# Optimization experiments

Hardware: AMD Instinct MI355X
Metric: run time of the kernel (lower is better)

The kernel has to match this reference:

```python
import jax, jax.numpy as jnp
import numpy as np

B, S, D_IN, D_HID, D_LAT = 64, 1024, 256, 512, 128
GRU_DIMS = [D_LAT, 256, 128]
D_OUT = 2
EPS_BN = 1e-5
EPS_LN = 1e-5


def _lin(key, out_d, in_d):
    k1, k2 = jax.random.split(key)
    s = 1.0 / np.sqrt(in_d)
    return (jax.random.uniform(k1, (out_d, in_d), jnp.float32, -s, s),
            jax.random.uniform(k2, (out_d,), jnp.float32, -s, s))


def setup_inputs() -> dict:
    key = jax.random.key(0)
    ks = jax.random.split(key, 16)
    x = jax.random.normal(ks[0], (B, S, D_IN), jnp.float32)
    eps = jax.random.normal(ks[1], (B, S, D_LAT), jnp.float32)
    W1lv, b1lv = _lin(ks[2], D_HID, D_IN)
    W2lv, b2lv = _lin(ks[3], D_LAT, D_HID)
    Wmu, bmu = _lin(ks[4], D_LAT, D_IN)
    Wdec, bdec = _lin(ks[5], D_IN, D_LAT)
    # GRU layer 0: in=128 -> hid=256; layer 1: in=256 -> hid=128
    Wih0, bih0 = _lin(ks[6], 3 * GRU_DIMS[1], GRU_DIMS[0])
    Whh0, bhh0 = _lin(ks[7], 3 * GRU_DIMS[1], GRU_DIMS[1])
    Wih1, bih1 = _lin(ks[8], 3 * GRU_DIMS[2], GRU_DIMS[1])
    Whh1, bhh1 = _lin(ks[9], 3 * GRU_DIMS[2], GRU_DIMS[2])
    fc_W, fc_b = _lin(ks[10], D_OUT, GRU_DIMS[2])
    return dict(
        x=x, eps=eps,
        W1lv=W1lv, b1lv=b1lv, W2lv=W2lv, b2lv=b2lv, Wmu=Wmu, bmu=bmu,
        bn_g=jnp.ones((D_LAT,), jnp.float32), bn_b=jnp.zeros((D_LAT,), jnp.float32),
        bn_rm=jnp.zeros((D_LAT,), jnp.float32), bn_rv=jnp.ones((D_LAT,), jnp.float32),
        Wdec=Wdec, bdec=bdec,
        Wih0=Wih0, Whh0=Whh0, bih0=bih0, bhh0=bhh0,
        Wih1=Wih1, Whh1=Whh1, bih1=bih1, bhh1=bhh1,
        ln_g0=jnp.ones((GRU_DIMS[1],), jnp.float32), ln_b0=jnp.zeros((GRU_DIMS[1],), jnp.float32),
        ln_g1=jnp.ones((GRU_DIMS[2],), jnp.float32), ln_b1=jnp.zeros((GRU_DIMS[2],), jnp.float32),
        fc_W=fc_W, fc_b=fc_b,
    )


def _gru_cell(x, h, Wih, Whh, bih, bhh):
    gi = x @ Wih.T + bih                      # [B, 3H]
    gh = h @ Whh.T + bhh
    ir, iz, inn = jnp.split(gi, 3, axis=-1)
    hr, hz, hn = jnp.split(gh, 3, axis=-1)
    r = jax.nn.sigmoid(ir + hr)
    zg = jax.nn.sigmoid(iz + hz)
    n = jnp.tanh(inn + r * hn)
    return (1.0 - zg) * n + zg * h


def _layernorm(h, g, b):
    m = jnp.mean(h, axis=-1, keepdims=True)
    v = jnp.var(h, axis=-1, keepdims=True)
    return (h - m) * jax.lax.rsqrt(v + EPS_LN) * g + b


def reference(x, eps, W1lv, b1lv, W2lv, b2lv, Wmu, bmu, bn_g, bn_b, bn_rm, bn_rv,
              Wdec, bdec, Wih0, Whh0, bih0, bhh0, Wih1, Whh1, bih1, bhh1,
              ln_g0, ln_b0, ln_g1, ln_b1, fc_W, fc_b):
    # --- Encoder ---
    xl = jnp.log(jax.nn.softplus(x))                       # [B,S,D_IN]
    h_enc = jax.nn.relu(xl @ W1lv.T + b1lv)                # [B,S,D_HID]
    logvar = h_enc @ W2lv.T + b2lv                         # [B,S,D_LAT]
    mu = xl @ Wmu.T + bmu                                  # [B,S,D_LAT]
    # BatchNorm1d over latent channel (eval mode, running stats)
    mu = (mu - bn_rm) * jax.lax.rsqrt(bn_rv + EPS_BN) * bn_g + bn_b
    mu = jnp.clip(mu, -10.0, 10.0)
    # --- Reparameterize ---
    z = mu + eps * jnp.exp(0.5 * logvar)                   # [B,S,D_LAT]
    # --- Decoder ---
    x_recon = jnp.exp(z @ Wdec.T + bdec)                   # [B,S,D_IN]
    # --- Stacked GRUCell + LayerNorm over time ---
    batch = x.shape[0]
    h0 = jnp.zeros((batch, GRU_DIMS[1]), z.dtype)
    h1 = jnp.zeros((batch, GRU_DIMS[2]), z.dtype)

    def step(carry, z_t):
        h0, h1 = carry
        h0 = _layernorm(_gru_cell(z_t, h0, Wih0, Whh0, bih0, bhh0), ln_g0, ln_b0)
        h1 = _layernorm(_gru_cell(h0, h1, Wih1, Whh1, bih1, bhh1), ln_g1, ln_b1)
        return (h0, h1), None

    (h0, h1), _ = jax.lax.scan(step, (h0, h1), jnp.swapaxes(z, 0, 1))
    # fc head (dropout is identity in eval mode); output_series=False
    v = h1 @ fc_W.T + fc_b                                 # [B, D_OUT]
    return (v, x_recon, mu, logvar)
```

## Files before the change

### kernel.cpp

```cpp
#include <hip/hip_runtime.h>
#include <cstdint>

#define TOKENS 65536

#define WS_XL    0ULL
#define WS_HENC  67108864ULL
#define WS_GI0   0ULL
#define WS_XBUF0 201326592ULL
#define WS_XBUF1 (201326592ULL + 131072ULL)
#define WS_CNT   (201326592ULL + 196608ULL)
#define WS_MUS   (201326592ULL + 229376ULL)
#define WS_MUT   (201326592ULL + 229888ULL)
#define WS_NEED  (201326592ULL + 230400ULL)
#define CNT_STRIDE 64

__global__ void k_prep(const float* __restrict__ bmu, const float* __restrict__ bng,
                       const float* __restrict__ bnb, const float* __restrict__ bnrm,
                       const float* __restrict__ bnrv,
                       float* __restrict__ mus, float* __restrict__ mut)
{
    int j = threadIdx.x;
    if (j < 128) {
        float s = bng[j] / sqrtf(bnrv[j] + 1e-5f);
        mus[j] = s;
        mut[j] = bmu[j] * s + bnb[j] - bnrm[j] * s;
    }
}

__global__ void k_xl(const float* __restrict__ x, float* __restrict__ xl, int n4)
{
    int i = blockIdx.x * blockDim.x + threadIdx.x;
    if (i >= n4) return;
    float4 v = ((const float4*)x)[i];
    float4 o;
    o.x = logf(v.x > 20.f ? v.x : log1pf(expf(v.x)));
    o.y = logf(v.y > 20.f ? v.y : log1pf(expf(v.y)));
    o.z = logf(v.z > 20.f ? v.z : log1pf(expf(v.z)));
    o.w = logf(v.w > 20.f ? v.w : log1pf(expf(v.w)));
    ((float4*)xl)[i] = o;
}

template<int EPI, int AZ>
__global__ __launch_bounds__(256) void k_gemm_f32(
    const float* __restrict__ A, const float* __restrict__ W,
    const float* __restrict__ svec, const float* __restrict__ tvec,
    float* __restrict__ C, int N, int K,
    const float* __restrict__ ZMU, const float* __restrict__ ZLV, const float* __restrict__ ZEP)
{
    __shared__ float As[32][132];
    __shared__ float Ws[32][132];
    const int tid = threadIdx.x;
    const int tx = tid & 15, ty = tid >> 4;
    const int m0 = blockIdx.x * 128;
    const int n0 = blockIdx.y * 128;
    float acc[8][8];
#pragma unroll
    for (int i = 0; i < 8; ++i)
#pragma unroll
        for (int j = 0; j < 8; ++j) acc[i][j] = 0.f;

    for (int k0 = 0; k0 < K; k0 += 32) {
#pragma unroll
        for (int it = 0; it < 4; ++it) {
            int id = tid + 256 * it;
            int r = id >> 3, c4 = id & 7;
            float4 av;
            if constexpr (AZ) {
                size_t idx = (size_t)(m0 + r) * K + k0 + c4 * 4;
                float4 m4 = *(const float4*)(ZMU + idx);
                float4 l4 = *(const float4*)(ZLV + idx);
                float4 e4 = *(const float4*)(ZEP + idx);
                av.x = m4.x + e4.x * expf(0.5f * l4.x);
                av.y = m4.y + e4.y * expf(0.5f * l4.y);
                av.z = m4.z + e4.z * expf(0.5f * l4.z);
                av.w = m4.w + e4.w * expf(0.5f * l4.w);
            } else {
                av = *(const float4*)(A + (size_t)(m0 + r) * K + k0 + c4 * 4);
            }
            float4 wv = *(const float4*)(W + (size_t)(n0 + r) * K + k0 + c4 * 4);
            As[c4*4+0][r] = av.x; As[c4*4+1][r] = av.y; As[c4*4+2][r] = av.z; As[c4*4+3][r] = av.w;
            Ws[c4*4+0][r] = wv.x; Ws[c4*4+1][r] = wv.y; Ws[c4*4+2][r] = wv.z; Ws[c4*4+3][r] = wv.w;
        }
        __syncthreads();
#pragma unroll
        for (int k = 0; k < 32; ++k) {
            float4 a0 = *(const float4*)&As[k][ty*8];
            float4 a1 = *(const float4*)&As[k][ty*8+4];
            float4 w0 = *(const float4*)&Ws[k][tx*8];
            float4 w1 = *(const float4*)&Ws[k][tx*8+4];
            float ar[8] = {a0.x,a0.y,a0.z,a0.w,a1.x,a1.y,a1.z,a1.w};
            float wr[8] = {w0.x,w0.y,w0.z,w0.w,w1.x,w1.y,w1.z,w1.w};
#pragma unroll
            for (int i = 0; i < 8; ++i)
#pragma unroll
                for (int j = 0; j < 8; ++j) acc[i][j] += ar[i] * wr[j];
        }
        __syncthreads();
    }
#pragma unroll
    for (int i = 0; i < 8; ++i) {
        size_t m = (size_t)m0 + ty*8 + i;
#pragma unroll
        for (int j4 = 0; j4 < 2; ++j4) {
            float o[4];
#pragma unroll
            for (int j = 0; j < 4; ++j) {
                int col = n0 + tx*8 + j4*4 + j;
                float v = acc[i][j4*4+j];
                if (svec) v *= svec[col];
                v += tvec[col];
                if constexpr (EPI == 1) v = fmaxf(v, 0.f);
                if constexpr (EPI == 2) v = fminf(fmaxf(v, -10.f), 10.f);
                if constexpr (EPI == 3) v = expf(v);
                o[j] = v;
            }
            *(float4*)(C + m * N + n0 + tx*8 + j4*4) = *(float4*)o;
        }
    }
}

__device__ __forceinline__ void xstore(float* p, float v) {
    __hip_atomic_store(p, v, __ATOMIC_RELAXED, __HIP_MEMORY_SCOPE_AGENT);
}
__device__ __forceinline__ float xload(const float* p) {
    return __hip_atomic_load(p, __ATOMIC_RELAXED, __HIP_MEMORY_SCOPE_AGENT);
}
__device__ __forceinline__ void xsync(unsigned* cb, unsigned tgt) {
    asm volatile("s_waitcnt vmcnt(0)" ::: "memory");
    __hip_atomic_fetch_add(cb, 1u, __ATOMIC_RELAXED, __HIP_MEMORY_SCOPE_AGENT);
    int guard = 0;
    while (__hip_atomic_load(cb, __ATOMIC_RELAXED, __HIP_MEMORY_SCOPE_AGENT) < tgt) {
        __builtin_amdgcn_s_sleep(2);
        if (++guard > (1 << 17)) break;
    }
    asm volatile("" ::: "memory");
}

__global__ __launch_bounds__(256)
__attribute__((amdgpu_waves_per_eu(1, 1)))
void k_scan0(const float* gi0, const float* wh0, const float* bhh0,
             const float* lg0, const float* lb0,
             float* h0s, float* xbuf, unsigned* cnt)
{
    const int xcd  = blockIdx.x & 7;
    const int slot = blockIdx.x >> 3;
    const int b    = xcd * 8 + (slot >> 2);
    const int q    = slot & 3;
    const int tid = threadIdx.x;
    const int lane = tid & 63;
    const int wvi  = tid >> 6;

    __shared__ float s_h[256];
    __shared__ float s_g[192];
    __shared__ float s_r1[4], s_r2[4];

    int row = 0;
    if (tid < 192)
        row = (tid < 64) ? (64*q + tid)
            : (tid < 128) ? (256 + 64*q + (tid-64))
                          : (512 + 64*q + (tid-128));
    float4 wr[64];
    float bA = 0.f;
    if (tid < 192) {
        const float4* p = (const float4*)(wh0 + (size_t)row * 256);
#pragma unroll
        for (int i = 0; i < 64; ++i) wr[i] = p[i];
        bA = bhh0[row];
    }
    const float gv = lg0[tid], bv = lb0[tid];
    s_h[tid] = 0.f;
    __syncthreads();

    const float* gbase = gi0 + (size_t)b * 1024 * 768;
    float* hb = h0s + (size_t)b * 1024 * 256;
    unsigned* cb = cnt + (size_t)b * CNT_STRIDE;

    for (int t = 0; t < 1024; ++t) {
        float gr = 0.f, gz = 0.f, gn = 0.f;
        if (tid >= 192) {
            const float* gt = gbase + (size_t)t * 768;
            int u = 64*q + (tid - 192);
            gr = gt[u]; gz = gt[256 + u]; gn = gt[512 + u];
        } else {
            float a0 = bA, a1 = 0.f, a2 = 0.f, a3 = 0.f;
            const float4* H = (const float4*)s_h;
#pragma unroll
            for (int i = 0; i < 64; ++i) {
                float4 h4 = H[i];
                a0 += wr[i].x * h4.x; a1 += wr[i].y * h4.y;
                a2 += wr[i].z * h4.z; a3 += wr[i].w * h4.w;
            }
            s_g[tid] = (a0 + a1) + (a2 + a3);
        }
        __syncthreads();
        float* xw = xbuf + (((size_t)b * 2 + (t & 1)) * 4 + q) * 64;
        if (tid >= 192) {
            int g = tid - 192;
            int u = 64*q + g;
            float r  = 1.f / (1.f + expf(-(gr + s_g[g])));
            float zg = 1.f / (1.f + expf(-(gz + s_g[64 + g])));
            float nn = tanhf(gn + r * s_g[128 + g]);
            float hn = (1.f - zg) * nn + zg * s_h[u];
            xstore(&xw[g], hn);
        }
        __syncthreads();
        if (tid == 0) xsync(cb, 4u * (unsigned)(t + 1));
        __syncthreads();
        const float* xr = xbuf + (((size_t)b * 2 + (t & 1)) * 4) * 64;
        float hn = xload(&xr[tid]);
        float sum = hn;
#pragma unroll
        for (int o = 32; o > 0; o >>= 1) sum += __shfl_xor(sum, o);
        if (lane == 0) s_r1[wvi] = sum;
        __syncthreads();
        float m = (s_r1[0] + s_r1[1] + s_r1[2] + s_r1[3]) * (1.f / 256.f);
        float d = hn - m;
        float ss = d * d;
#pragma unroll
        for (int o = 32; o > 0; o >>= 1) ss += __shfl_xor(ss, o);
        if (lane == 0) s_r2[wvi] = ss;
        __syncthreads();
        float va = (s_r2[0] + s_r2[1] + s_r2[2] + s_r2[3]) * (1.f / 256.f);
        float rs = 1.f / sqrtf(va + 1e-5f);
        float hl = d * rs * gv + bv;
        s_h[tid] = hl;
        if (q == 0) hb[(size_t)t * 256 + tid] = hl;
        __syncthreads();
    }
}

__global__ __launch_bounds__(256)
__attribute__((amdgpu_waves_per_eu(1, 1)))
void k_scan1(const float* h0s, const float* wi1, const float* wh1,
             const float* bih1, const float* bhh1,
             const float* lg1, const float* lb1,
             const float* fcW, const float* fcb,
             float* vout, float* xbuf, unsigned* cnt)
{
    const int xcd  = blockIdx.x & 7;
    const int slot = blockIdx.x >> 3;
    const int b    = xcd * 8 + (slot >> 2);
    const int q    = slot & 3;
    const int tid = threadIdx.x;
    const int lane = tid & 63;
    const int wvi  = tid >> 6;

    __shared__ float s_x[2][256];
    __shared__ float s_h[128];
    __shared__ float s_g[768];
    __shared__ float s_r1[2], s_r2[2];

    float4 wr[64];
    float bB = 0.f;
    if (tid < 96) {
        int jj = tid;
        int row = (jj < 32) ? (32*q + jj) : (jj < 64) ? (128 + 32*q + (jj-32)) : (256 + 32*q + (jj-64));
        const float4* p = (const float4*)(wi1 + (size_t)row * 256);
#pragma unroll
        for (int i = 0; i < 64; ++i) wr[i] = p[i];
        bB = bih1[row];
    } else if (tid < 192) {
        int jj = tid - 96;
        int row = (jj < 32) ? (32*q + jj) : (jj < 64) ? (128 + 32*q + (jj-32)) : (256 + 32*q + (jj-64));
        const float4* p = (const float4*)(wh1 + (size_t)row * 128);
#pragma unroll
        for (int i = 0; i < 32; ++i) wr[i] = p[i];
        bB = bhh1[row];
    }
    float gv = 0.f, bv = 0.f;
    if (tid < 128) { gv = lg1[tid]; bv = lb1[tid]; s_h[tid] = 0.f; }
    const float4* xb4 = (const float4*)(h0s + (size_t)b * 1024 * 256);
    if (tid < 64) ((float4*)s_x[0])[tid] = xb4[tid];
    __syncthreads();

    unsigned* cb = cnt + (size_t)b * CNT_STRIDE;

    for (int t = 0; t < 1024; ++t) {
        const int cur = t & 1, nxt = cur ^ 1;
        float4 st0, st1;
        const bool stg = (tid >= 224) && (t + 1 < 1024);
        if (stg) {
            int k = tid - 224;
            st0 = xb4[(size_t)(t+1) * 64 + k];
            st1 = xb4[(size_t)(t+1) * 64 + k + 32];
        }
        if (tid < 96) {
            float a0 = bB, a1 = 0.f, a2 = 0.f, a3 = 0.f;
            const float4* X = (const float4*)s_x[cur];
#pragma unroll
            for (int i = 0; i < 64; ++i) {
                float4 h4 = X[i];
                a0 += wr[i].x * h4.x; a1 += wr[i].y * h4.y;
                a2 += wr[i].z * h4.z; a3 += wr[i].w * h4.w;
            }
            s_g[tid] = (a0 + a1) + (a2 + a3);
        } else if (tid < 192) {
            float a0 = bB, a1 = 0.f, a2 = 0.f, a3 = 0.f;
            const float4* Hh = (const float4*)s_h;
#pragma unroll
            for (int i = 0; i < 32; ++i) {
                float4 h4 = Hh[i];
                a0 += wr[i].x * h4.x; a1 += wr[i].y * h4.y;
                a2 += wr[i].z * h4.z; a3 += wr[i].w * h4.w;
            }
            s_g[96 + (tid - 96)] = (a0 + a1) + (a2 + a3);
        }
        __syncthreads();
        float* xw = xbuf + (((size_t)b * 2 + (t & 1)) * 4 + q) * 32;
        if (tid >= 192 && tid < 224) {
            int g = tid - 192;
            int u = 32*q + g;
            float r  = 1.f / (1.f + expf(-(s_g[g]      + s_g[96 + g])));
            float zg = 1.f / (1.f + expf(-(s_g[32 + g] + s_g[128 + g])));
            float nn = tanhf(s_g[64 + g] + r * s_g[160 + g]);
            float hn = (1.f - zg) * nn + zg * s_h[u];
            xstore(&xw[g], hn);
        } else if (stg) {
            int k = tid - 224;
            ((float4*)s_x[nxt])[k]      = st0;
            ((float4*)s_x[nxt])[k + 32] = st1;
        }
        __syncthreads();
        if (tid == 0) xsync(cb, 4u * (unsigned)(t + 1));
        __syncthreads();
        const float* xr = xbuf + (((size_t)b * 2 + (t & 1)) * 4) * 32;
        float hn = 0.f, d = 0.f;
        if (tid < 128) {
            hn = xload(&xr[tid]);
            float sum = hn;
#pragma unroll
            for (int o = 32; o > 0; o >>= 1) sum += __shfl_xor(sum, o);
            if (lane == 0) s_r1[wvi] = sum;
        }
        __syncthreads();
        if (tid < 128) {
            float m = (s_r1[0] + s_r1[1]) * (1.f / 128.f);
            d = hn - m;
            float ss = d * d;
#pragma unroll
            for (int o = 32; o > 0; o >>= 1) ss += __shfl_xor(ss, o);
            if (lane == 0) s_r2[wvi] = ss;
        }
        __syncthreads();
        if (tid < 128) {
            float va = (s_r2[0] + s_r2[1]) * (1.f / 128.f);
            float rs = 1.f / sqrtf(va + 1e-5f);
            float hl = d * rs * gv + bv;
            s_h[tid] = hl;
        }
        __syncthreads();
    }
    float p0 = 0.f, p1 = 0.f;
    if (tid < 128) {
        float hold = s_h[tid];
        p0 = fcW[tid] * hold;
        p1 = fcW[128 + tid] * hold;
#pragma unroll
        for (int o = 32; o > 0; o >>= 1) { p0 += __shfl_xor(p0, o); p1 += __shfl_xor(p1, o); }
        if (lane == 0) { s_r1[wvi] = p0; s_r2[wvi] = p1; }
    }
    __syncthreads();
    if (tid == 0 && q == 0) {
        vout[b * 2 + 0] = s_r1[0] + s_r1[1] + fcb[0];
        vout[b * 2 + 1] = s_r2[0] + s_r2[1] + fcb[1];
    }
}

extern "C" void kernel_launch(void* const* d_in, const int* in_sizes, int n_in,
                              void* d_out, int out_size, void* d_ws, size_t ws_size,
                              hipStream_t stream)
{
    const float* x     = (const float*)d_in[0];
    const float* eps   = (const float*)d_in[1];
    const float* W1lv  = (const float*)d_in[2];
    const float* b1lv  = (const float*)d_in[3];
    const float* W2lv  = (const float*)d_in[4];
    const float* b2lv  = (const float*)d_in[5];
    const float* Wmu   = (const float*)d_in[6];
    const float* bmu   = (const float*)d_in[7];
    const float* bn_g  = (const float*)d_in[8];
    const float* bn_b  = (const float*)d_in[9];
    const float* bn_rm = (const float*)d_in[10];
    const float* bn_rv = (const float*)d_in[11];
    const float* Wdec  = (const float*)d_in[12];
    const float* bdec  = (const float*)d_in[13];
    const float* Wih0  = (const float*)d_in[14];
    const float* Whh0  = (const float*)d_in[15];
    const float* bih0  = (const float*)d_in[16];
    const float* bhh0  = (const float*)d_in[17];
    const float* Wih1  = (const float*)d_in[18];
    const float* Whh1  = (const float*)d_in[19];
    const float* bih1  = (const float*)d_in[20];
    const float* bhh1  = (const float*)d_in[21];
    const float* ln_g0 = (const float*)d_in[22];
    const float* ln_b0 = (const float*)d_in[23];
    const float* ln_g1 = (const float*)d_in[24];
    const float* ln_b1 = (const float*)d_in[25];
    const float* fc_W  = (const float*)d_in[26];
    const float* fc_b  = (const float*)d_in[27];

    float* out   = (float*)d_out;
    float* v_out = out;
    float* xrec  = out + 128;
    float* mu    = out + 128 + 16777216;
    float* lv    = out + 128 + 16777216 + 8388608;
    float* H0S   = xrec;

    if (ws_size < WS_NEED) return;
    char* ws = (char*)d_ws;
    float*    XL    = (float*)(ws + WS_XL);
    float*    HENC  = (float*)(ws + WS_HENC);
    float*    GI0   = (float*)(ws + WS_GI0);
    float*    XBUF0 = (float*)(ws + WS_XBUF0);
    float*    XBUF1 = (float*)(ws + WS_XBUF1);
    unsigned* CNT0  = (unsigned*)(ws + WS_CNT);
    unsigned* CNT1  = CNT0 + 64 * CNT_STRIDE;
    float*    MUS   = (float*)(ws + WS_MUS);
    float*    MUT   = (float*)(ws + WS_MUT);

    k_prep<<<1, 128, 0, stream>>>(bmu, bn_g, bn_b, bn_rm, bn_rv, MUS, MUT);
    k_xl<<<16384, 256, 0, stream>>>(x, XL, 4194304);
    k_gemm_f32<1,0><<<dim3(512, 4), 256, 0, stream>>>(XL,   W1lv, nullptr, b1lv, HENC, 512, 256, nullptr, nullptr, nullptr);
    k_gemm_f32<0,0><<<dim3(512, 1), 256, 0, stream>>>(HENC, W2lv, nullptr, b2lv, lv,   128, 512, nullptr, nullptr, nullptr);
    k_gemm_f32<2,0><<<dim3(512, 1), 256, 0, stream>>>(XL,   Wmu,  MUS,     MUT,  mu,   128, 256, nullptr, nullptr, nullptr);
    k_gemm_f32<0,1><<<dim3(512, 6), 256, 0, stream>>>(nullptr, Wih0, nullptr, bih0, GI0, 768, 128, mu, lv, eps);
    hipMemsetAsync(CNT0, 0, 32768, stream);
    k_scan0<<<256, 256, 0, stream>>>(GI0, Whh0, bhh0, ln_g0, ln_b0, H0S, XBUF0, CNT0);
    k_scan1<<<256, 256, 0, stream>>>(H0S, Wih1, Whh1, bih1, bhh1, ln_g1, ln_b1, fc_W, fc_b, v_out, XBUF1, CNT1);
    k_gemm_f32<3,1><<<dim3(512, 2), 256, 0, stream>>>(nullptr, Wdec, nullptr, bdec, xrec, 256, 128, mu, lv, eps);
}
```

Before: 8.466 ms.

## Replace counter barrier with tagged per-element flags in GRU scan exchange

The per-timestep cross-block exchange in both GRU scan kernels now packs each hidden value together with a timestep tag into a 64-bit word, and consumers poll their own element until the tag matches. This removes the global atomic counter, the thread-0 spin, and two block-wide barriers per step. Workgroup barriers are also replaced with a lighter s_barrier that waits only on LDS counters. The risks are more polling traffic and the loss of double buffering: a fast block could overwrite a slot before a slower peer has read it, though the tag check limits what a reader will accept.

```diff
diff --git a/kernel.cpp b/kernel.cpp
--- a/kernel.cpp
+++ b/kernel.cpp
@@ -1,5 +1,7 @@
 #include <hip/hip_runtime.h>
 #include <cstdint>
+
+typedef unsigned long long u64;
 
 #define TOKENS 65536
 
@@ -8,11 +10,9 @@
 #define WS_GI0   0ULL
 #define WS_XBUF0 201326592ULL
 #define WS_XBUF1 (201326592ULL + 131072ULL)
-#define WS_CNT   (201326592ULL + 196608ULL)
-#define WS_MUS   (201326592ULL + 229376ULL)
-#define WS_MUT   (201326592ULL + 229888ULL)
-#define WS_NEED  (201326592ULL + 230400ULL)
-#define CNT_STRIDE 64
+#define WS_MUS   (201326592ULL + 196608ULL)
+#define WS_MUT   (201326592ULL + 197120ULL)
+#define WS_NEED  (201326592ULL + 197632ULL)
 
 __global__ void k_prep(const float* __restrict__ bmu, const float* __restrict__ bng,
                        const float* __restrict__ bnb, const float* __restrict__ bnrm,
@@ -119,28 +119,29 @@
     }
 }
 
-__device__ __forceinline__ void xstore(float* p, float v) {
-    __hip_atomic_store(p, v, __ATOMIC_RELAXED, __HIP_MEMORY_SCOPE_AGENT);
-}
-__device__ __forceinline__ float xload(const float* p) {
-    return __hip_atomic_load(p, __ATOMIC_RELAXED, __HIP_MEMORY_SCOPE_AGENT);
-}
-__device__ __forceinline__ void xsync(unsigned* cb, unsigned tgt) {
-    asm volatile("s_waitcnt vmcnt(0)" ::: "memory");
-    __hip_atomic_fetch_add(cb, 1u, __ATOMIC_RELAXED, __HIP_MEMORY_SCOPE_AGENT);
-    int guard = 0;
-    while (__hip_atomic_load(cb, __ATOMIC_RELAXED, __HIP_MEMORY_SCOPE_AGENT) < tgt) {
-        __builtin_amdgcn_s_sleep(2);
-        if (++guard > (1 << 17)) break;
-    }
-    asm volatile("" ::: "memory");
+__device__ __forceinline__ void tstore(u64* p, float v, unsigned tag) {
+    u64 w = ((u64)tag << 32) | (u64)__builtin_bit_cast(unsigned, v);
+    __hip_atomic_store(p, w, __ATOMIC_RELAXED, __HIP_MEMORY_SCOPE_AGENT);
+}
+__device__ __forceinline__ float tpoll(const u64* p, unsigned tag) {
+    u64 w = 0; int guard = 0;
+    do {
+        w = __hip_atomic_load(p, __ATOMIC_RELAXED, __HIP_MEMORY_SCOPE_AGENT);
+        if ((unsigned)(w >> 32) == tag) break;
+        __builtin_amdgcn_s_sleep(1);
+    } while (++guard < (1 << 17));
+    return __builtin_bit_cast(float, (unsigned)w);
+}
+__device__ __forceinline__ void rbar() {
+    asm volatile("s_waitcnt lgkmcnt(0)" ::: "memory");
+    __builtin_amdgcn_s_barrier();
 }
 
 __global__ __launch_bounds__(256)
 __attribute__((amdgpu_waves_per_eu(1, 1)))
 void k_scan0(const float* gi0, const float* wh0, const float* bhh0,
              const float* lg0, const float* lb0,
-             float* h0s, float* xbuf, unsigned* cnt)
+             float* h0s, u64* xbuf)
 {
     const int xcd  = blockIdx.x & 7;
     const int slot = blockIdx.x >> 3;
@@ -173,7 +174,7 @@
 
     const float* gbase = gi0 + (size_t)b * 1024 * 768;
     float* hb = h0s + (size_t)b * 1024 * 256;
-    unsigned* cb = cnt + (size_t)b * CNT_STRIDE;
+    u64* xb = xbuf + (size_t)b * 256;
 
     for (int t = 0; t < 1024; ++t) {
         float gr = 0.f, gz = 0.f, gn = 0.f;
@@ -192,8 +193,7 @@
             }
             s_g[tid] = (a0 + a1) + (a2 + a3);
         }
-        __syncthreads();
-        float* xw = xbuf + (((size_t)b * 2 + (t & 1)) * 4 + q) * 64;
+        rbar();
         if (tid >= 192) {
             int g = tid - 192;
             int u = 64*q + g;
@@ -201,31 +201,27 @@
             float zg = 1.f / (1.f + expf(-(gz + s_g[64 + g])));
             float nn = tanhf(gn + r * s_g[128 + g]);
             float hn = (1.f - zg) * nn + zg * s_h[u];
-            xstore(&xw[g], hn);
-        }
-        __syncthreads();
-        if (tid == 0) xsync(cb, 4u * (unsigned)(t + 1));
-        __syncthreads();
-        const float* xr = xbuf + (((size_t)b * 2 + (t & 1)) * 4) * 64;
-        float hn = xload(&xr[tid]);
+            tstore(&xb[u], hn, (unsigned)(t + 1));
+        }
+        float hn = tpoll(&xb[tid], (unsigned)(t + 1));
         float sum = hn;
 #pragma unroll
         for (int o = 32; o > 0; o >>= 1) sum += __shfl_xor(sum, o);
         if (lane == 0) s_r1[wvi] = sum;
-        __syncthreads();
+        rbar();
         float m = (s_r1[0] + s_r1[1] + s_r1[2] + s_r1[3]) * (1.f / 256.f);
         float d = hn - m;
         float ss = d * d;
 #pragma unroll
         for (int o = 32; o > 0; o >>= 1) ss += __shfl_xor(ss, o);
         if (lane == 0) s_r2[wvi] = ss;
-        __syncthreads();
+        rbar();
         float va = (s_r2[0] + s_r2[1] + s_r2[2] + s_r2[3]) * (1.f / 256.f);
         float rs = 1.f / sqrtf(va + 1e-5f);
         float hl = d * rs * gv + bv;
         s_h[tid] = hl;
         if (q == 0) hb[(size_t)t * 256 + tid] = hl;
-        __syncthreads();
+        rbar();
     }
 }
 
@@ -235,7 +231,7 @@
              const float* bih1, const float* bhh1,
              const float* lg1, const float* lb1,
              const float* fcW, const float* fcb,
-             float* vout, float* xbuf, unsigned* cnt)
+             float* vout, u64* xbuf)
 {
     const int xcd  = blockIdx.x & 7;
     const int slot = blockIdx.x >> 3;
@@ -247,7 +243,7 @@
 
     __shared__ float s_x[2][256];
     __shared__ float s_h[128];
-    __shared__ float s_g[768];
+    __shared__ float s_g[192];
     __shared__ float s_r1[2], s_r2[2];
 
     float4 wr[64];
@@ -273,7 +269,7 @@
     if (tid < 64) ((float4*)s_x[0])[tid] = xb4[tid];
     __syncthreads();
 
-    unsigned* cb = cnt + (size_t)b * CNT_STRIDE;
+    u64* xb = xbuf + (size_t)b * 128;
 
     for (int t = 0; t < 1024; ++t) {
         const int cur = t & 1, nxt = cur ^ 1;
@@ -305,8 +301,7 @@
             }
             s_g[96 + (tid - 96)] = (a0 + a1) + (a2 + a3);
         }
-        __syncthreads();
-        float* xw = xbuf + (((size_t)b * 2 + (t & 1)) * 4 + q) * 32;
+        rbar();
         if (tid >= 192 && tid < 224) {
             int g = tid - 192;
             int u = 32*q + g;
@@ -314,25 +309,21 @@
             float zg = 1.f / (1.f + expf(-(s_g[32 + g] + s_g[128 + g])));
             float nn = tanhf(s_g[64 + g] + r * s_g[160 + g]);
             float hn = (1.f - zg) * nn + zg * s_h[u];
-            xstore(&xw[g], hn);
+            tstore(&xb[u], hn, (unsigned)(t + 1));
         } else if (stg) {
             int k = tid - 224;
             ((float4*)s_x[nxt])[k]      = st0;
             ((float4*)s_x[nxt])[k + 32] = st1;
         }
-        __syncthreads();
-        if (tid == 0) xsync(cb, 4u * (unsigned)(t + 1));
-        __syncthreads();
-        const float* xr = xbuf + (((size_t)b * 2 + (t & 1)) * 4) * 32;
         float hn = 0.f, d = 0.f;
         if (tid < 128) {
-            hn = xload(&xr[tid]);
+            hn = tpoll(&xb[tid], (unsigned)(t + 1));
             float sum = hn;
 #pragma unroll
             for (int o = 32; o > 0; o >>= 1) sum += __shfl_xor(sum, o);
             if (lane == 0) s_r1[wvi] = sum;
         }
-        __syncthreads();
+        rbar();
         if (tid < 128) {
             float m = (s_r1[0] + s_r1[1]) * (1.f / 128.f);
             d = hn - m;
@@ -341,14 +332,14 @@
             for (int o = 32; o > 0; o >>= 1) ss += __shfl_xor(ss, o);
             if (lane == 0) s_r2[wvi] = ss;
         }
-        __syncthreads();
+        rbar();
         if (tid < 128) {
             float va = (s_r2[0] + s_r2[1]) * (1.f / 128.f);
             float rs = 1.f / sqrtf(va + 1e-5f);
             float hl = d * rs * gv + bv;
             s_h[tid] = hl;
         }
-        __syncthreads();
+        rbar();
     }
     float p0 = 0.f, p1 = 0.f;
     if (tid < 128) {
@@ -408,15 +399,13 @@
 
     if (ws_size < WS_NEED) return;
     char* ws = (char*)d_ws;
-    float*    XL    = (float*)(ws + WS_XL);
-    float*    HENC  = (float*)(ws + WS_HENC);
-    float*    GI0   = (float*)(ws + WS_GI0);
-    float*    XBUF0 = (float*)(ws + WS_XBUF0);
-    float*    XBUF1 = (float*)(ws + WS_XBUF1);
-    unsigned* CNT0  = (unsigned*)(ws + WS_CNT);
-    unsigned* CNT1  = CNT0 + 64 * CNT_STRIDE;
-    float*    MUS   = (float*)(ws + WS_MUS);
-    float*    MUT   = (float*)(ws + WS_MUT);
+    float* XL    = (float*)(ws + WS_XL);
+    float* HENC  = (float*)(ws + WS_HENC);
+    float* GI0   = (float*)(ws + WS_GI0);
+    u64*   XBUF0 = (u64*)(ws + WS_XBUF0);
+    u64*   XBUF1 = (u64*)(ws + WS_XBUF1);
+    float* MUS   = (float*)(ws + WS_MUS);
+    float* MUT   = (float*)(ws + WS_MUT);
 
     k_prep<<<1, 128, 0, stream>>>(bmu, bn_g, bn_b, bn_rm, bn_rv, MUS, MUT);
     k_xl<<<16384, 256, 0, stream>>>(x, XL, 4194304);
@@ -424,8 +413,8 @@
     k_gemm_f32<0,0><<<dim3(512, 1), 256, 0, stream>>>(HENC, W2lv, nullptr, b2lv, lv,   128, 512, nullptr, nullptr, nullptr);
     k_gemm_f32<2,0><<<dim3(512, 1), 256, 0, stream>>>(XL,   Wmu,  MUS,     MUT,  mu,   128, 256, nullptr, nullptr, nullptr);
     k_gemm_f32<0,1><<<dim3(512, 6), 256, 0, stream>>>(nullptr, Wih0, nullptr, bih0, GI0, 768, 128, mu, lv, eps);
-    hipMemsetAsync(CNT0, 0, 32768, stream);
-    k_scan0<<<256, 256, 0, stream>>>(GI0, Whh0, bhh0, ln_g0, ln_b0, H0S, XBUF0, CNT0);
-    k_scan1<<<256, 256, 0, stream>>>(H0S, Wih1, Whh1, bih1, bhh1, ln_g1, ln_b1, fc_W, fc_b, v_out, XBUF1, CNT1);
+    hipMemsetAsync(XBUF0, 0, 196608, stream);
+    k_scan0<<<256, 256, 0, stream>>>(GI0, Whh0, bhh0, ln_g0, ln_b0, H0S, XBUF0);
+    k_scan1<<<256, 256, 0, stream>>>(H0S, Wih1, Whh1, bih1, bhh1, ln_g1, ln_b1, fc_W, fc_b, v_out, XBUF1);
     k_gemm_f32<3,1><<<dim3(512, 2), 256, 0, stream>>>(nullptr, Wdec, nullptr, bdec, xrec, 256, 128, mu, lv, eps);
 }
```

New measurement: 8.001 ms. 1.06x faster.
